# Optimization experiments

Hardware: AMD Instinct MI355X
Metric: run time of the kernel (lower is better)

## Reference

```python
import jax, jax.numpy as jnp
import numpy as np

# Qwen3.5 GatedDeltaNet dims
B, T, HID = 2, 2048, 2048
HK, HV, DK, DV, KW = 16, 32, 128, 128, 4   # k-heads, v-heads, head dims, conv kernel
R = HV // HK                                # GQA repeat factor = 2
KEY_DIM = HK * DK                           # 2048
VAL_DIM = HV * DV                           # 4096
CONV_DIM = 2 * KEY_DIM + VAL_DIM            # 8192
EPS = 1e-6


def setup_inputs() -> dict:
    key = jax.random.key(0)
    ks = jax.random.split(key, 10)
    w = lambda k, shape, s=0.02: (jax.random.normal(k, shape) * s).astype(jnp.float32)
    A = jax.random.uniform(ks[8], (HV,), minval=1e-3, maxval=16.0)
    return {
        "hidden_states": jax.random.normal(ks[0], (B, T, HID), jnp.float32),
        "W_qkv": w(ks[1], (HID, CONV_DIM)),
        "W_z": w(ks[2], (HID, VAL_DIM)),
        "W_b": w(ks[3], (HID, HV)),
        "W_a": w(ks[4], (HID, HV)),
        "conv_w": w(ks[5], (CONV_DIM, KW), 0.5),   # depthwise causal conv taps
        "dt_bias": jnp.ones((HV,), jnp.float32),
        "A_log": jnp.log(A).astype(jnp.float32),
        "norm_weight": jnp.ones((DV,), jnp.float32),
        "W_out": w(ks[9], (VAL_DIM, HID)),
    }


def _forward(hidden_states, W_qkv, W_z, W_b, W_a, conv_w, dt_bias, A_log, norm_weight, W_out):
    x = hidden_states
    # --- projections ---
    qkv = x @ W_qkv                                    # [B,T,CONV_DIM]
    z = x @ W_z                                        # [B,T,VAL_DIM]
    beta = jax.nn.sigmoid(x @ W_b)                     # [B,T,HV]
    alpha = x @ W_a                                    # [B,T,HV]
    g = -jnp.exp(A_log) * jax.nn.softplus(alpha + dt_bias)  # [B,T,HV] (log-decay <= 0)

    # --- fix_query_key_value_ordering: per-k-head interleaved layout ---
    qkv = qkv.reshape(B, T, HK, 2 * DK + R * DV)
    q, k, v = jnp.split(qkv, [DK, 2 * DK], axis=3)
    mixed = jnp.concatenate([q.reshape(B, T, -1), k.reshape(B, T, -1), v.reshape(B, T, -1)], axis=-1)

    # --- causal depthwise short conv (kernel 4) + SiLU ---
    xp = jnp.pad(mixed, ((0, 0), (KW - 1, 0), (0, 0)))
    conv = sum(conv_w[:, i] * xp[:, i:i + T, :] for i in range(KW))
    conv = jax.nn.silu(conv)

    q, k, v = jnp.split(conv, [KEY_DIM, 2 * KEY_DIM], axis=-1)
    q = q.reshape(B, T, HK, DK)
    k = k.reshape(B, T, HK, DK)
    v = v.reshape(B, T, HV, DV)
    gate = z.reshape(B, T, HV, DV)

    # GQA: repeat q,k heads to match v heads
    q = jnp.repeat(q, R, axis=2)                       # [B,T,HV,DK]
    k = jnp.repeat(k, R, axis=2)

    # l2-norm q,k (use_qk_l2norm_in_kernel=True) and default scale 1/sqrt(DK)
    q = q / jnp.sqrt(jnp.sum(q * q, axis=-1, keepdims=True) + 1e-6)
    k = k / jnp.sqrt(jnp.sum(k * k, axis=-1, keepdims=True) + 1e-6)
    q = q * (DK ** -0.5)

    # --- gated delta rule recurrence (scan over time) ---
    # state S: [B,HV,DK,DV];  S_t = a_t*S_{t-1} + k_t (beta_t*(v_t - (a_t*S_{t-1})^T k_t))^T
    def step(S, inp):
        qt, kt, vt, gt, bt = inp                       # [B,HV,DK],[B,HV,DK],[B,HV,DV],[B,HV],[B,HV]
        S = S * jnp.exp(gt)[:, :, None, None]
        kv = jnp.einsum('bhk,bhkv->bhv', kt, S)
        delta = bt[..., None] * (vt - kv)              # [B,HV,DV]
        S = S + kt[..., None] * delta[:, :, None, :]
        o = jnp.einsum('bhk,bhkv->bhv', qt, S)
        return S, o

    tfirst = lambda a: jnp.moveaxis(a, 1, 0)           # [T,B,...]
    S0 = jnp.zeros((B, HV, DK, DV), q.dtype)
    _, o = jax.lax.scan(step, S0, (tfirst(q), tfirst(k), tfirst(v), tfirst(g), tfirst(beta)))
    o = jnp.moveaxis(o, 0, 1)                          # [B,T,HV,DV]

    # --- gated RMSNorm: rmsnorm(o) * silu(gate) * weight ---
    var = jnp.mean(o * o, axis=-1, keepdims=True)
    o = o * jax.lax.rsqrt(var + EPS)
    o = o * jax.nn.silu(gate)
    o = o * norm_weight

    return o.reshape(B, T, VAL_DIM) @ W_out            # [B,T,HID]


def reference(hidden_states, W_qkv, W_z, W_b, W_a, conv_w, dt_bias, A_log, norm_weight, W_out):
    return _forward(hidden_states, W_qkv, W_z, W_b, W_a, conv_w, dt_bias, A_log, norm_weight, W_out)
```

## Files before the change

kernel.cpp:

```cpp
#include <hip/hip_runtime.h>


#define T_LEN 2048
#define MROWS 4096

typedef __bf16 bf16x8 __attribute__((ext_vector_type(8)));
typedef float f32x4 __attribute__((ext_vector_type(4)));

#define MFMA(a, b, c) __builtin_amdgcn_mfma_f32_16x16x32_bf16((a), (b), (c), 0, 0, 0)

__device__ __forceinline__ unsigned short f2bf(float f) {
  unsigned int u = __float_as_uint(f);
  unsigned int r = (u + 0x7fffu + ((u >> 16) & 1u)) >> 16;
  return (unsigned short)r;
}
__device__ __forceinline__ float bf2f(unsigned short u) {
  return __uint_as_float(((unsigned int)u) << 16);
}
__device__ __forceinline__ void gload_lds16(const void* g, void* l) {
  __builtin_amdgcn_global_load_lds(
      (const __attribute__((address_space(1))) unsigned int*)g,
      (__attribute__((address_space(3))) unsigned int*)l, 16, 0, 0);
}

__global__ __launch_bounds__(256) void transpose_f2b(const float* __restrict__ src,
                                                     unsigned short* __restrict__ dst,
                                                     int R, int C) {
  __shared__ float tile[32][33];
  int tx = threadIdx.x & 31, ty = threadIdx.x >> 5;
  int c0 = blockIdx.x * 32, r0 = blockIdx.y * 32;
  #pragma unroll
  for (int i = ty; i < 32; i += 8)
    tile[i][tx] = src[(size_t)(r0 + i) * C + c0 + tx];
  __syncthreads();
  #pragma unroll
  for (int i = ty; i < 32; i += 8)
    dst[(size_t)(c0 + i) * R + r0 + tx] = f2bf(tile[tx][i]);
}

__global__ __launch_bounds__(256) void transpose_multi(const float* __restrict__ Wqkv,
                                                       const float* __restrict__ Wz,
                                                       const float* __restrict__ Wb,
                                                       const float* __restrict__ Wa,
                                                       const float* __restrict__ x,
                                                       unsigned short* __restrict__ WallT,
                                                       unsigned short* __restrict__ WbaT,
                                                       unsigned short* __restrict__ x_bf) {
  int bid = blockIdx.x;
  if (bid >= 24704) {
    int i = (bid - 24704) * 256 + threadIdx.x;
    float4 v = ((const float4*)x)[i];
    ushort4 o;
    o.x = f2bf(v.x); o.y = f2bf(v.y); o.z = f2bf(v.z); o.w = f2bf(v.w);
    ((ushort4*)x_bf)[i] = o;
    return;
  }
  const float* src; unsigned short* dst; int C, cx, ry;
  if (bid < 16384)                 { src = Wqkv; dst = WallT; C = 8192; cx = bid & 255; ry = bid >> 8; }
  else if ((bid -= 16384) < 8192)  { src = Wz; dst = WallT + (size_t)8192 * 2048; C = 4096; cx = bid & 127; ry = bid >> 7; }
  else if ((bid -= 8192) < 64)     { src = Wb; dst = WbaT; C = 32; cx = 0; ry = bid; }
  else { bid -= 64;                  src = Wa; dst = WbaT + (size_t)32 * 2048; C = 32; cx = 0; ry = bid; }
  const int R = 2048;
  __shared__ float tile[32][33];
  int tx = threadIdx.x & 31, ty = threadIdx.x >> 5;
  int c0 = cx * 32, r0 = ry * 32;
  #pragma unroll
  for (int i = ty; i < 32; i += 8)
    if (c0 + tx < C) tile[i][tx] = src[(size_t)(r0 + i) * C + c0 + tx];
  __syncthreads();
  #pragma unroll
  for (int i = ty; i < 32; i += 8)
    if (c0 + i < C) dst[(size_t)(c0 + i) * R + r0 + tx] = f2bf(tile[tx][i]);
}

template <int OUTBF>
__global__ __launch_bounds__(512, 2) void gemm8p(const unsigned short* __restrict__ A, int lda,
                                                 const unsigned short* __restrict__ Bt, int ldb,
                                                 void* __restrict__ Cv, int ldc,
                                                 int Nsplit, void* __restrict__ Cv2, int ldc2,
                                                 int M, int N, int K) {
  __shared__ unsigned short lds[65536];

  const int mtiles = M >> 8;
  const int nwg = gridDim.x, orig = blockIdx.x;
  const int q = nwg >> 3, r = nwg & 7;
  const int xcd = orig & 7, idx = orig >> 3;
  const int swz = (xcd < r ? xcd * (q + 1) : r * (q + 1) + (xcd - r) * q) + idx;
  const int m0 = (swz % mtiles) * 256;
  const int n0 = (swz / mtiles) * 256;

  const int tid = threadIdx.x, lane = tid & 63, wv = tid >> 6;
  const int wm = wv >> 2, wn = wv & 3;
  const int l15 = lane & 15, l4 = lane >> 4;

  f32x4 acc[8][4];
  #pragma unroll
  for (int i = 0; i < 8; i++)
    #pragma unroll
    for (int j = 0; j < 4; j++) acc[i][j] = f32x4{0.f, 0.f, 0.f, 0.f};

  const int NT = K >> 6;

  auto SHALF = [&](int t, int op, int h) {
    unsigned short* base = lds + (t & 1) * 32768 + op * 16384 + h * 8192;
    const unsigned short* G = op ? Bt : A;
    const int ld = op ? ldb : lda;
    const int r0g = (op ? n0 : m0) + h * 128;
    const int k0 = t << 6;
    #pragma unroll
    for (int is = 0; is < 2; is++) {
      int ow = is * 8192 + wv * 1024;
      int o = ow + lane * 16;
      int row = o >> 7, colB = o & 127;
      int scol = colB ^ ((row & 7) << 4);
      gload_lds16(G + (size_t)(r0g + row) * ld + k0 + (scol >> 1), base + (ow >> 1));
    }
  };

  bf16x8 aF[4][2], bF[2][2];
  auto RD_A = [&](int t, int qm) {
    const unsigned short* base = lds + (t & 1) * 32768 + qm * 8192;
    #pragma unroll
    for (int mi = 0; mi < 4; mi++) {
      int ra = wm * 64 + mi * 16 + l15;
      int sw = (ra & 7) << 4;
      #pragma unroll
      for (int kh = 0; kh < 2; kh++) {
        int colB = kh * 64 + l4 * 16;
        aF[mi][kh] = *(const bf16x8*)(base + ra * 64 + ((colB ^ sw) >> 1));
      }
    }
  };
  auto RD_B = [&](int t, int qn) {
    const unsigned short* base = lds + (t & 1) * 32768 + 16384 + qn * 8192;
    #pragma unroll
    for (int ni = 0; ni < 2; ni++) {
      int rb = wn * 32 + ni * 16 + l15;
      int sw = (rb & 7) << 4;
      #pragma unroll
      for (int kh = 0; kh < 2; kh++) {
        int colB = kh * 64 + l4 * 16;
        bF[ni][kh] = *(const bf16x8*)(base + rb * 64 + ((colB ^ sw) >> 1));
      }
    }
  };
  auto COMPUTE = [&](int qm, int qn) {
    __builtin_amdgcn_s_setprio(1);
    #pragma unroll
    for (int mi = 0; mi < 4; mi++)
      #pragma unroll
      for (int ni = 0; ni < 2; ni++)
        #pragma unroll
        for (int kh = 0; kh < 2; kh++)
          acc[qm * 4 + mi][qn * 2 + ni] =
              MFMA(aF[mi][kh], bF[ni][kh], acc[qm * 4 + mi][qn * 2 + ni]);
    __builtin_amdgcn_s_setprio(0);
  };
  auto SBAR = [&]() {
    __builtin_amdgcn_sched_barrier(0);
    __builtin_amdgcn_s_barrier();
    __builtin_amdgcn_sched_barrier(0);
  };

  SHALF(0, 0, 0); SHALF(0, 1, 0); SHALF(0, 1, 1); SHALF(0, 0, 1);
  asm volatile("s_waitcnt vmcnt(4)" ::: "memory");
  SBAR();

  for (int t = 0; t < NT; t++) {
    const bool lastT = (t + 1 >= NT);
    RD_A(t, 0); RD_B(t, 0);
    if (!lastT) SHALF(t + 1, 0, 0);
    COMPUTE(0, 0);
    if (!lastT) asm volatile("s_waitcnt vmcnt(4)" ::: "memory");
    else        asm volatile("s_waitcnt vmcnt(2)" ::: "memory");
    SBAR();
    RD_B(t, 1);
    if (!lastT) SHALF(t + 1, 1, 0);
    COMPUTE(0, 1);
    if (!lastT) asm volatile("s_waitcnt vmcnt(4)" ::: "memory");
    else        asm volatile("s_waitcnt vmcnt(0)" ::: "memory");
    SBAR();
    RD_A(t, 1);
    if (!lastT) SHALF(t + 1, 1, 1);
    COMPUTE(1, 1);
    RD_B(t, 0);
    if (!lastT) SHALF(t + 1, 0, 1);
    COMPUTE(1, 0);
    if (!lastT) {
      asm volatile("s_waitcnt vmcnt(4)" ::: "memory");
      SBAR();
    }
  }

  #pragma unroll
  for (int i = 0; i < 8; i++) {
    int grow = m0 + (i >> 2) * 128 + wm * 64 + (i & 3) * 16 + l4 * 4;
    #pragma unroll
    for (int j = 0; j < 4; j++) {
      int gcol = n0 + (j >> 1) * 128 + wn * 32 + (j & 1) * 16 + l15;
      if (OUTBF) {
        if (gcol < Nsplit) {
          unsigned short* cp = (unsigned short*)Cv + (size_t)grow * ldc + gcol;
          #pragma unroll
          for (int rr = 0; rr < 4; rr++) cp[(size_t)rr * ldc] = f2bf(acc[i][j][rr]);
        } else {
          unsigned short* cp = (unsigned short*)Cv2 + (size_t)grow * ldc2 + (gcol - Nsplit);
          #pragma unroll
          for (int rr = 0; rr < 4; rr++) cp[(size_t)rr * ldc2] = f2bf(acc[i][j][rr]);
        }
      } else {
        float* cp = (float*)Cv + (size_t)grow * ldc + gcol;
        #pragma unroll
        for (int rr = 0; rr < 4; rr++) cp[(size_t)rr * ldc] = acc[i][j][rr];
      }
    }
  }
}

template <int OUTBF, int BN>
__global__ __launch_bounds__(512, 2) void gemm256(const unsigned short* __restrict__ A, int lda,
                                                  const unsigned short* __restrict__ Bt, int ldb,
                                                  void* __restrict__ Cv, int ldc,
                                                  int M, int N, int K) {
  constexpr int BUFSZ = 16384 + BN * 64;
  constexpr int BISS = BN / 64;
  constexpr int IS = 4 + BISS;
  constexpr int WMv = (BN == 256) ? 2 : 4;
  constexpr int MSUB = 256 / (WMv * 16);
  constexpr int MSPAN = 256 / WMv;

  __shared__ unsigned short lds[2 * BUFSZ];

  const int mtiles = M >> 8;
  const int nwg = gridDim.x;
  const int orig = blockIdx.x;
  const int q = nwg >> 3, r = nwg & 7;
  const int xcd = orig & 7, idx = orig >> 3;
  const int swz = (xcd < r ? xcd * (q + 1) : r * (q + 1) + (xcd - r) * q) + idx;
  const int m0 = (swz % mtiles) * 256;
  const int n0 = (swz / mtiles) * BN;

  const int tid = threadIdx.x, lane = tid & 63, wv = tid >> 6;
  const int wm = (BN == 256) ? (wv >> 2) : (wv >> 1);
  const int wn = (BN == 256) ? (wv & 3) : (wv & 1);
  const int l15 = lane & 15, l4 = lane >> 4;

  f32x4 acc[MSUB][4];
  #pragma unroll
  for (int i = 0; i < MSUB; i++)
    #pragma unroll
    for (int j = 0; j < 4; j++) acc[i][j] = f32x4{0.f, 0.f, 0.f, 0.f};

  const int NT = K >> 6;

  auto STAGE = [&](int kt) {
    unsigned short* base = lds + (kt & 1) * BUFSZ;
    const int k0 = kt << 6;
    #pragma unroll
    for (int is = 0; is < 4; is++) {
      int ow = is * 8192 + wv * 1024;
      int o = ow + lane * 16;
      int row = o >> 7, colB = o & 127;
      int scol = colB ^ ((row & 7) << 4);
      gload_lds16(A + (size_t)(m0 + row) * lda + k0 + (scol >> 1), base + (ow >> 1));
    }
    #pragma unroll
    for (int is = 0; is < BISS; is++) {
      int ow = is * 8192 + wv * 1024;
      int o = ow + lane * 16;
      int row = o >> 7, colB = o & 127;
      int scol = colB ^ ((row & 7) << 4);
      gload_lds16(Bt + (size_t)(n0 + row) * ldb + k0 + (scol >> 1), base + 16384 + (ow >> 1));
    }
  };

  STAGE(0);
  if (NT > 1) STAGE(1);
  if constexpr (IS == 8) asm volatile("s_waitcnt vmcnt(8)" ::: "memory");
  else                   asm volatile("s_waitcnt vmcnt(6)" ::: "memory");
  __builtin_amdgcn_sched_barrier(0);
  __builtin_amdgcn_s_barrier();
  __builtin_amdgcn_sched_barrier(0);

  for (int t = 0; t < NT; t++) {
    const unsigned short* Abuf = lds + (t & 1) * BUFSZ;
    const unsigned short* Bbuf = Abuf + 16384;
    bf16x8 bF[4][2];
    #pragma unroll
    for (int n = 0; n < 4; n++) {
      int rb = wn * 64 + n * 16 + l15;
      int sw = (rb & 7) << 4;
      #pragma unroll
      for (int ks = 0; ks < 2; ks++) {
        int colB = (ks * 32 + l4 * 8) * 2;
        bF[n][ks] = *(const bf16x8*)(Bbuf + rb * 64 + ((colB ^ sw) >> 1));
      }
    }
    __builtin_amdgcn_s_setprio(1);
    #pragma unroll
    for (int m = 0; m < MSUB; m++) {
      int ra = wm * MSPAN + m * 16 + l15;
      int sw = (ra & 7) << 4;
      int c0b = l4 * 16;
      bf16x8 a0 = *(const bf16x8*)(Abuf + ra * 64 + ((c0b ^ sw) >> 1));
      bf16x8 a1 = *(const bf16x8*)(Abuf + ra * 64 + (((64 + c0b) ^ sw) >> 1));
      #pragma unroll
      for (int n = 0; n < 4; n++) {
        acc[m][n] = MFMA(a0, bF[n][0], acc[m][n]);
        acc[m][n] = MFMA(a1, bF[n][1], acc[m][n]);
      }
    }
    __builtin_amdgcn_s_setprio(0);
    __builtin_amdgcn_sched_barrier(0);
    __builtin_amdgcn_s_barrier();
    __builtin_amdgcn_sched_barrier(0);
    if (t + 2 < NT) STAGE(t + 2);
    if (t + 1 < NT) {
      if (t + 2 < NT) {
        if constexpr (IS == 8) asm volatile("s_waitcnt vmcnt(8)" ::: "memory");
        else                   asm volatile("s_waitcnt vmcnt(6)" ::: "memory");
      } else {
        asm volatile("s_waitcnt vmcnt(0)" ::: "memory");
      }
      __builtin_amdgcn_sched_barrier(0);
      __builtin_amdgcn_s_barrier();
      __builtin_amdgcn_sched_barrier(0);
    }
  }

  #pragma unroll
  for (int m = 0; m < MSUB; m++) {
    int grow = m0 + wm * MSPAN + m * 16 + l4 * 4;
    #pragma unroll
    for (int n = 0; n < 4; n++) {
      int gcol = n0 + wn * 64 + n * 16 + l15;
      if (OUTBF) {
        unsigned short* cp = (unsigned short*)Cv + (size_t)grow * ldc + gcol;
        #pragma unroll
        for (int rr = 0; rr < 4; rr++) cp[(size_t)rr * ldc] = f2bf(acc[m][n][rr]);
      } else {
        float* cp = (float*)Cv + (size_t)grow * ldc + gcol;
        #pragma unroll
        for (int rr = 0; rr < 4; rr++) cp[(size_t)rr * ldc] = acc[m][n][rr];
      }
    }
  }
}

__global__ __launch_bounds__(256) void gemm_ba(const unsigned short* __restrict__ A, int lda,
                                               const unsigned short* __restrict__ Bt, int ldb,
                                               const float* __restrict__ A_log,
                                               const float* __restrict__ dt_bias,
                                               unsigned short* __restrict__ betab,
                                               float* __restrict__ g,
                                               int M, int K) {
  __shared__ unsigned short As[128 * 64];
  __shared__ unsigned short Bs[128 * 64];
  const int tid = threadIdx.x, lane = tid & 63, wv = tid >> 6;
  const int wr = wv >> 1, wc = wv & 1;
  const int m0 = blockIdx.y * 128, n0 = 0;
  const int lrow8 = lane >> 3;
  const int lk8 = (lane & 7) * 8;

  f32x4 acc[4][4];
  #pragma unroll
  for (int i = 0; i < 4; i++)
    #pragma unroll
    for (int j = 0; j < 4; j++) acc[i][j] = f32x4{0.f, 0.f, 0.f, 0.f};

  for (int k0 = 0; k0 < K; k0 += 64) {
    #pragma unroll
    for (int j = 0; j < 4; ++j) {
      int chunk = j * 4 + wv;
      int r = chunk * 8 + lrow8;
      gload_lds16(A + (size_t)(m0 + r) * lda + k0 + lk8, (void*)(As + chunk * 512));
      gload_lds16(Bt + (size_t)(n0 + r) * ldb + k0 + lk8, (void*)(Bs + chunk * 512));
    }
    __syncthreads();
    #pragma unroll
    for (int half = 0; half < 2; ++half) {
      int ko = half * 32 + (lane >> 4) * 8;
      bf16x8 af[4], bfr[4];
      #pragma unroll
      for (int i = 0; i < 4; i++) {
        int ra = wr * 64 + i * 16 + (lane & 15);
        af[i] = *(const bf16x8*)(As + ra * 64 + ko);
        int rb = wc * 64 + i * 16 + (lane & 15);
        bfr[i] = *(const bf16x8*)(Bs + rb * 64 + ko);
      }
      #pragma unroll
      for (int i = 0; i < 4; i++)
        #pragma unroll
        for (int j = 0; j < 4; j++)
          acc[i][j] = MFMA(af[i], bfr[j], acc[i][j]);
    }
    __syncthreads();
  }
  int cr4 = (lane >> 4) * 4;
  int cc = lane & 15;
  #pragma unroll
  for (int i = 0; i < 4; i++) {
    int row = m0 + wr * 64 + i * 16 + cr4;
    #pragma unroll
    for (int j = 0; j < 4; j++) {
      int col = wc * 64 + j * 16 + cc;
      if (col < 64) {
        #pragma unroll
        for (int r = 0; r < 4; r++) {
          int erow = row + r;
          float a = acc[i][j][r];
          if (col < 32) {
            betab[(size_t)erow * 32 + col] = f2bf(1.f / (1.f + expf(-a)));
          } else {
            int hvv = col - 32;
            float xg = a + dt_bias[hvv];
            float sp = (xg > 20.f) ? xg : log1pf(expf(xg));
            g[(size_t)erow * 32 + hvv] = -expf(A_log[hvv]) * sp;
          }
        }
      }
    }
  }
}

__global__ __launch_bounds__(256) void conv_kernel(const unsigned short* __restrict__ qkv,
                                                   const float* __restrict__ conv_w,
                                                   unsigned short* __restrict__ out) {
  const int seg = blockIdx.x, tt = blockIdx.y, b = blockIdx.z;
  const int tid = threadIdx.x;
  const int c0 = seg * 128;
  const bool isq = seg < 16;
  int scb;
  if (isq) scb = seg * 512;
  else if (seg < 32) scb = (seg - 16) * 512 + 128;
  else scb = ((seg - 32) >> 1) * 512 + 256 + ((seg - 32) & 1) * 128;

  __shared__ unsigned short raw[35][136];
  __shared__ float cw[4][132];

  for (int i = tid; i < 512; i += 256) {
    int cl = i >> 2, tap = i & 3;
    cw[tap][cl] = conv_w[(size_t)(c0 + cl) * 4 + tap];
  }
  const int t0 = tt * 32;
  for (int i = tid; i < 560; i += 256) {
    int row = i >> 4, col = (i & 15) * 8;
    int gt = t0 - 3 + row;
    uint4 v = make_uint4(0u, 0u, 0u, 0u);
    if (gt >= 0) v = *(const uint4*)(qkv + (size_t)(b * T_LEN + gt) * 8192 + scb + col);
    *(uint4*)(&raw[row][col]) = v;
  }
  __syncthreads();
  const int s = tid >> 3, dg = tid & 7;
  union RawU { uint4 v[2]; unsigned short h[16]; };
  RawU u[4];
  #pragma unroll
  for (int i = 0; i < 4; i++) {
    const uint4* p = (const uint4*)&raw[s + i][dg * 16];
    u[i].v[0] = p[0]; u[i].v[1] = p[1];
  }
  float vals[16]; float ss = 0.f;
  #pragma unroll
  for (int j = 0; j < 16; j++) {
    float a = 0.f;
    #pragma unroll
    for (int i = 0; i < 4; i++) a = fmaf(cw[i][dg * 16 + j], bf2f(u[i].h[j]), a);
    a = a / (1.f + expf(-a));
    vals[j] = a; ss += a * a;
  }
  if (seg < 32) {
    ss += __shfl_xor(ss, 1); ss += __shfl_xor(ss, 2); ss += __shfl_xor(ss, 4);
    float sc = rsqrtf(ss + 1e-6f);
    if (isq) sc *= 0.08838834764831845f;
    #pragma unroll
    for (int j = 0; j < 16; j++) vals[j] *= sc;
  }
  union { uint4 v[2]; unsigned short h[16]; } ov;
  #pragma unroll
  for (int j = 0; j < 16; j++) ov.h[j] = f2bf(vals[j]);
  unsigned short* op = out + (size_t)(b * T_LEN + t0 + s) * 8192 + c0 + dg * 16;
  *(uint4*)(op) = ov.v[0];
  *(uint4*)(op + 8) = ov.v[1];
}

__global__ __launch_bounds__(256) void prep_kernel(const unsigned short* __restrict__ conv,
                                                   const float* __restrict__ g,
                                                   const unsigned short* __restrict__ betab,
                                                   unsigned short* __restrict__ M1g,
                                                   unsigned short* __restrict__ M2g,
                                                   unsigned char* __restrict__ vecs) {
  const int c = blockIdx.x, bh = blockIdx.y;
  const int b = bh >> 5, hv = bh & 31, hk = hv >> 1;
  const int bhc = bh * 32 + c;
  const int tid = threadIdx.x, lane = tid & 63, wv = tid >> 6;
  const int r0 = b * T_LEN + c * 64;
  const int l15 = lane & 15, l4 = lane >> 4;

  __shared__ unsigned short Kb[128 * 72];
  __shared__ unsigned short QbX[64 * 136];
  __shared__ unsigned short Lbf[64 * 72];
  __shared__ unsigned short Pb[64 * 72];
  __shared__ unsigned short WT[3 * 16 * 40];
  __shared__ float Gs[64], SCs[64], BLs[64];

  unsigned short* Qb = QbX;
  unsigned short* XTb = QbX;
  unsigned short* Xdrow = QbX + 4608;

  if (wv == 0) {
    float gt = g[(size_t)(r0 + lane) * 32 + hv];
    #pragma unroll
    for (int d = 1; d < 64; d <<= 1) {
      float o = __shfl_up(gt, (unsigned)d, 64);
      if (lane >= d) gt += o;
    }
    float GC = __shfl(gt, 63, 64);
    float lam = expf(gt);
    float beta = bf2f(betab[(size_t)(r0 + lane) * 32 + hv]);
    Gs[lane] = gt;
    SCs[lane] = expf(GC - gt);
    BLs[lane] = beta;
    unsigned short* vb16 = (unsigned short*)(vecs + (size_t)bhc * 272);
    vb16[lane] = f2bf(beta * lam);
    vb16[64 + lane] = f2bf(lam);
    if (lane == 0) *(float*)(vecs + (size_t)bhc * 272 + 256) = expf(GC);
  }
  const unsigned short* Kg = conv + (size_t)r0 * 8192 + 2048 + hk * 128;
  const unsigned short* Qg = conv + (size_t)r0 * 8192 + hk * 128;
  for (int u = tid; u < 1024; u += 256) {
    int row = u >> 4, col = (u & 15) * 8;
    *(uint4*)(&Kb[row * 136 + col]) = *(const uint4*)(Kg + (size_t)row * 8192 + col);
    *(uint4*)(&Qb[row * 136 + col]) = *(const uint4*)(Qg + (size_t)row * 8192 + col);
  }
  __syncthreads();

  {
    f32x4 akk[4], aqk[4];
    #pragma unroll
    for (int st = 0; st < 4; st++) { akk[st] = f32x4{0,0,0,0}; aqk[st] = f32x4{0,0,0,0}; }
    int trow = wv * 16 + l15;
    int klo = l4 * 8;
    #pragma unroll
    for (int ks = 0; ks < 4; ks++) {
      int ko = ks * 32 + klo;
      bf16x8 ak = *(const bf16x8*)(&Kb[trow * 136 + ko]);
      bf16x8 aq = *(const bf16x8*)(&Qb[trow * 136 + ko]);
      #pragma unroll
      for (int st = 0; st < 4; st++) {
        bf16x8 bk = *(const bf16x8*)(&Kb[(st * 16 + l15) * 136 + ko]);
        akk[st] = MFMA(ak, bk, akk[st]);
        aqk[st] = MFMA(aq, bk, aqk[st]);
      }
    }
    int orow = wv * 16 + l4 * 4;
    int oc = l15;
    #pragma unroll
    for (int st = 0; st < 4; st++)
      #pragma unroll
      for (int r = 0; r < 4; r++) {
        int t = orow + r, ssv = st * 16 + oc;
        float e = expf(fminf(Gs[t] - Gs[ssv], 0.f));
        Lbf[t * 72 + ssv] = f2bf((ssv < t) ? BLs[t] * e * akk[st][r] : 0.f);
        Pb[t * 72 + ssv] = f2bf((ssv <= t) ? e * aqk[st][r] : 0.f);
      }
  }
  __syncthreads();

  unsigned short ktv[32];
  {
    int dk = tid >> 1, tb = (tid & 1) * 32;
    #pragma unroll
    for (int i = 0; i < 32; i++)
      ktv[i] = f2bf(bf2f(Kb[(tb + i) * 136 + dk]) * SCs[tb + i]);
    for (int u = tid; u < 896; u += 256) {
      *(uint4*)(&QbX[u * 8]) = make_uint4(0u, 0u, 0u, 0u);
    }
    for (int u = tid; u < 240; u += 256) {
      *(uint4*)(&WT[u * 8]) = make_uint4(0u, 0u, 0u, 0u);
    }
  }
  __syncthreads();

  {
    int dk = tid >> 1, tb = (tid & 1) * 32;
    #pragma unroll
    for (int i = 0; i < 32; i++) Kb[dk * 72 + tb + i] = ktv[i];
  }
  {
    const int w16 = wv * 16;
    const int cc = l15;
    float xr[16];
    #pragma unroll
    for (int t = 0; t < 16; t++) {
      float acc = (cc == t) ? 1.f : 0.f;
      union { uint4 v[2]; unsigned short h[16]; } rw;
      const uint4* p = (const uint4*)(&Lbf[(w16 + t) * 72 + w16]);
      rw.v[0] = p[0]; rw.v[1] = p[1];
      #pragma unroll
      for (int s = 0; s < 16; s++) {
        if (s < t) acc = fmaf(-bf2f(rw.h[s]), xr[s], acc);
      }
      xr[t] = acc;
    }
    if (lane < 16) {
      #pragma unroll
      for (int t = 0; t < 16; t++) {
        unsigned short v = f2bf(xr[t]);
        XTb[(w16 + cc) * 72 + w16 + t] = v;
        Xdrow[wv * 640 + t * 40 + cc] = v;
      }
    }
  }
  __syncthreads();

  if (wv < 3) {
    const int j = wv;
    for (int i = j + 1; i < 4; i++) {
      f32x4 w_ = f32x4{0.f, 0.f, 0.f, 0.f};
      #pragma unroll
      for (int ks = 0; ks < 2; ks++) {
        int so = ks * 32 + l4 * 8;
        bf16x8 af = *(const bf16x8*)(&Lbf[(i * 16 + l15) * 72 + so]);
        bf16x8 bfv = *(const bf16x8*)(&XTb[(j * 16 + l15) * 72 + so]);
        w_ = MFMA(af, bfv, w_);
      }
      #pragma unroll
      for (int r = 0; r < 4; r++)
        WT[j * 640 + l15 * 40 + l4 * 4 + r] = f2bf(-w_[r]);
      f32x4 xij = f32x4{0.f, 0.f, 0.f, 0.f};
      {
        bf16x8 af = *(const bf16x8*)(&Xdrow[i * 640 + l15 * 40 + l4 * 8]);
        bf16x8 bfv = *(const bf16x8*)(&WT[j * 640 + l15 * 40 + l4 * 8]);
        xij = MFMA(af, bfv, xij);
      }
      #pragma unroll
      for (int r = 0; r < 4; r++)
        XTb[(j * 16 + l15) * 72 + i * 16 + l4 * 4 + r] = f2bf(xij[r]);
    }
  }
  __syncthreads();

  for (int tt = wv * 12; tt < wv * 12 + 12; tt++) {
    f32x4 acc = f32x4{0, 0, 0, 0};
    const unsigned short* Abase;
    int mrow, jc;
    if (tt < 16) { mrow = (tt >> 2) * 16; jc = (tt & 3) * 16; Abase = Pb + mrow * 72; }
    else { int i2 = tt - 16; mrow = (i2 >> 2) * 16; jc = (i2 & 3) * 16; Abase = Kb + mrow * 72; }
    #pragma unroll
    for (int ks = 0; ks < 2; ks++) {
      int so = ks * 32 + l4 * 8;
      bf16x8 af = *(const bf16x8*)(Abase + l15 * 72 + so);
      bf16x8 bfv = *(const bf16x8*)(&XTb[(jc + l15) * 72 + so]);
      acc = MFMA(af, bfv, acc);
    }
    int ro = mrow + l4 * 4, co = jc + l15;
    if (tt < 16) {
      #pragma unroll
      for (int r = 0; r < 4; r++)
        M1g[(size_t)bhc * 4096 + (ro + r) * 64 + co] = f2bf(acc[r]);
    } else {
      #pragma unroll
      for (int r = 0; r < 4; r++)
        M2g[(size_t)bhc * 8192 + (ro + r) * 64 + co] = f2bf(acc[r]);
    }
  }
}

__global__ __launch_bounds__(512) void seq_kernel(unsigned short* __restrict__ conv,
                                                  const unsigned short* __restrict__ M1g,
                                                  const unsigned short* __restrict__ M2g,
                                                  const unsigned char* __restrict__ vecs,
                                                  const unsigned short* __restrict__ betab) {
  const int dvh = blockIdx.x * 64;
  const int bh = blockIdx.y;
  const int b = bh >> 5, hv = bh & 31, hk = hv >> 1;
  const int tid = threadIdx.x, lane = tid & 63, wv = tid >> 6;
  const int l15 = lane & 15, l4 = lane >> 4;

  __shared__ unsigned short Kb[64 * 136], Qb[64 * 136];
  __shared__ unsigned short Vb[64 * 72];
  __shared__ unsigned short S0T[64 * 136];
  __shared__ unsigned short rhsT[64 * 72];
  __shared__ unsigned short bts[64];

  f32x4 S[4];
  #pragma unroll
  for (int i = 0; i < 4; i++) S[i] = f32x4{0.f, 0.f, 0.f, 0.f};

  for (int i = tid; i < 1088; i += 512) *(uint4*)(&S0T[i * 8]) = make_uint4(0u, 0u, 0u, 0u);
  __syncthreads();

  const int trt = (wv >> 1) * 16;
  const int dsb = (wv & 1) * 32;
  const int dkb = wv * 16;

  for (int c = 0; c < 32; c++) {
    const int r0 = b * T_LEN + c * 64;
    const int bhc = bh * 32 + c;
    const unsigned char* vb = vecs + (size_t)bhc * 272;
    const unsigned short* vb16 = (const unsigned short*)vb;
    #pragma unroll
    for (int j = 0; j < 2; j++) {
      int u = j * 512 + tid;
      int row = u >> 4, col = (u & 15) * 8;
      uint4 kv = *(const uint4*)(conv + (size_t)(r0 + row) * 8192 + 2048 + hk * 128 + col);
      uint4 qv = *(const uint4*)(conv + (size_t)(r0 + row) * 8192 + hk * 128 + col);
      *(uint4*)(&Kb[row * 136 + col]) = kv;
      float lam = bf2f(vb16[64 + row]);
      union { uint4 u4; unsigned short h[8]; } qq; qq.u4 = qv;
      #pragma unroll
      for (int e = 0; e < 8; e++) qq.h[e] = f2bf(bf2f(qq.h[e]) * lam);
      *(uint4*)(&Qb[row * 136 + col]) = qq.u4;
    }
    {
      int row = tid >> 3, col = (tid & 7) * 8;
      *(uint4*)(&Vb[row * 72 + col]) =
          *(const uint4*)(conv + (size_t)(r0 + row) * 8192 + 4096 + hv * 128 + dvh + col);
      if (tid < 64) bts[tid] = betab[(size_t)(r0 + tid) * 32 + hv];
    }
    __syncthreads();
    #pragma unroll
    for (int dt = 0; dt < 2; dt++) {
      int dv0 = dsb + dt * 16;
      f32x4 acc = f32x4{0, 0, 0, 0};
      #pragma unroll
      for (int ks = 0; ks < 4; ks++) {
        int ko = ks * 32 + l4 * 8;
        bf16x8 af = *(const bf16x8*)(&Kb[(trt + l15) * 136 + ko]);
        bf16x8 bfv = *(const bf16x8*)(&S0T[(dv0 + l15) * 136 + ko]);
        acc = MFMA(af, bfv, acc);
      }
      #pragma unroll
      for (int r = 0; r < 4; r++) {
        int tl = trt + l4 * 4 + r;
        float beta = bf2f(bts[tl]);
        float bl = bf2f(vb16[tl]);
        float vv = bf2f(Vb[tl * 72 + dv0 + l15]);
        rhsT[(dv0 + l15) * 72 + tl] = f2bf(beta * vv - bl * acc[r]);
      }
    }
    __syncthreads();
    {
      const unsigned short* m1b = M1g + (size_t)bhc * 4096;
      #pragma unroll
      for (int dt = 0; dt < 2; dt++) {
        int dv0 = dsb + dt * 16;
        f32x4 acc = f32x4{0, 0, 0, 0};
        #pragma unroll
        for (int ks = 0; ks < 2; ks++) {
          int so = ks * 32 + l4 * 8;
          union { uint4 u4; bf16x8 h; } af;
          af.u4 = *(const uint4*)(m1b + (trt + l15) * 64 + so);
          bf16x8 bfv = *(const bf16x8*)(&rhsT[(dv0 + l15) * 72 + so]);
          acc = MFMA(af.h, bfv, acc);
        }
        #pragma unroll
        for (int ks = 0; ks < 4; ks++) {
          int ko = ks * 32 + l4 * 8;
          bf16x8 af = *(const bf16x8*)(&Qb[(trt + l15) * 136 + ko]);
          bf16x8 bfv = *(const bf16x8*)(&S0T[(dv0 + l15) * 136 + ko]);
          acc = MFMA(af, bfv, acc);
        }
        #pragma unroll
        for (int r = 0; r < 4; r++) {
          int t = r0 + trt + l4 * 4 + r;
          conv[(size_t)t * 8192 + 4096 + hv * 128 + dvh + dv0 + l15] = f2bf(acc[r]);
        }
      }
      float lamC = *(const float*)(vb + 256);
      const unsigned short* m2b = M2g + (size_t)bhc * 8192;
      #pragma unroll
      for (int dvt = 0; dvt < 4; dvt++) {
        f32x4 a = S[dvt];
        a[0] *= lamC; a[1] *= lamC; a[2] *= lamC; a[3] *= lamC;
        #pragma unroll
        for (int ks = 0; ks < 2; ks++) {
          int so = ks * 32 + l4 * 8;
          union { uint4 u4; bf16x8 h; } af;
          af.u4 = *(const uint4*)(m2b + (dkb + l15) * 64 + so);
          bf16x8 bfv = *(const bf16x8*)(&rhsT[(dvt * 16 + l15) * 72 + so]);
          a = MFMA(af.h, bfv, a);
        }
        S[dvt] = a;
      }
    }
    __syncthreads();
    #pragma unroll
    for (int dvt = 0; dvt < 4; dvt++)
      #pragma unroll
      for (int r = 0; r < 4; r++)
        S0T[(dvt * 16 + l15) * 136 + dkb + l4 * 4 + r] = f2bf(S[dvt][r]);
  }
}

__global__ __launch_bounds__(256) void rmsgate_kernel(unsigned short* __restrict__ conv,
                                                      const unsigned short* __restrict__ zg,
                                                      const float* __restrict__ nw) {
  int wid = blockIdx.x * 4 + (threadIdx.x >> 6);
  int lane = threadIdx.x & 63;
  int row = wid >> 5, hv = wid & 31;
  unsigned short* op = conv + (size_t)row * 8192 + 4096 + hv * 128;
  float o0 = bf2f(op[lane]), o1 = bf2f(op[64 + lane]);
  float ss = o0 * o0 + o1 * o1;
  #pragma unroll
  for (int m = 1; m < 64; m <<= 1) ss += __shfl_xor(ss, m);
  float r = rsqrtf(ss * (1.f / 128.f) + 1e-6f);
  const unsigned short* zp = zg + (size_t)row * 4096 + hv * 128;
  float g0 = bf2f(zp[lane]), g1 = bf2f(zp[64 + lane]);
  g0 = g0 / (1.f + expf(-g0));
  g1 = g1 / (1.f + expf(-g1));
  op[lane] = f2bf(o0 * r * g0 * nw[lane]);
  op[64 + lane] = f2bf(o1 * r * g1 * nw[64 + lane]);
}

extern "C" void kernel_launch(void* const* d_in, const int* in_sizes, int n_in,
                              void* d_out, int out_size, void* d_ws, size_t ws_size,
                              hipStream_t stream) {
  (void)in_sizes; (void)n_in; (void)out_size;
  const float* x       = (const float*)d_in[0];
  const float* W_qkv   = (const float*)d_in[1];
  const float* W_z     = (const float*)d_in[2];
  const float* W_b     = (const float*)d_in[3];
  const float* W_a     = (const float*)d_in[4];
  const float* conv_w  = (const float*)d_in[5];
  const float* dt_bias = (const float*)d_in[6];
  const float* A_log   = (const float*)d_in[7];
  const float* nw      = (const float*)d_in[8];
  const float* W_out   = (const float*)d_in[9];
  float* out = (float*)d_out;

  const size_t NEED = 169115648ULL;
  if (ws_size < NEED) return;

  char* ws = (char*)d_ws;
  unsigned short* WbaT   = (unsigned short*)(ws + 0);
  unsigned short* qkv_bf = (unsigned short*)(ws + 0);
  unsigned short* M1g    = (unsigned short*)(ws + 0);
  unsigned short* M2g    = (unsigned short*)(ws + 16777216);
  unsigned short* WoutT  = (unsigned short*)(ws + 0);
  unsigned short* zg     = (unsigned short*)(ws + 67108864);
  unsigned short* WallT  = (unsigned short*)(ws + 100663296);
  unsigned short* x_bf   = (unsigned short*)(ws + 100663296 + 50331648);
  unsigned short* convb  = (unsigned short*)(ws + 100663296);
  unsigned short* betab  = (unsigned short*)(ws + 167772160);
  float* gbuf            = (float*)(ws + 168034304);
  unsigned char* vecs    = (unsigned char*)(ws + 168558592);

  const int M = MROWS;

  transpose_multi<<<32896, 256, 0, stream>>>(W_qkv, W_z, W_b, W_a, x, WallT, WbaT, x_bf);

  gemm_ba<<<dim3(1, M / 128), 256, 0, stream>>>(x_bf, 2048, WbaT, 2048,
                                                A_log, dt_bias, betab, gbuf, M, 2048);

  gemm8p<1><<<768, 512, 0, stream>>>(x_bf, 2048, WallT, 2048,
                                     qkv_bf, 8192, 8192, zg, 4096, M, 12288, 2048);

  conv_kernel<<<dim3(64, 64, 2), 256, 0, stream>>>(qkv_bf, conv_w, convb);

  prep_kernel<<<dim3(32, 64), 256, 0, stream>>>(convb, gbuf, betab, M1g, M2g, vecs);

  seq_kernel<<<dim3(2, 64), 512, 0, stream>>>(convb, M1g, M2g, vecs, betab);

  rmsgate_kernel<<<32768, 256, 0, stream>>>(convb, zg, nw);

  transpose_f2b<<<dim3(2048 / 32, 4096 / 32), 256, 0, stream>>>(W_out, WoutT, 4096, 2048);
  gemm256<0, 128><<<256, 512, 0, stream>>>(convb + 4096, 8192, WoutT, 4096, out, 2048, M, 2048, 4096);
}
```

Before: 597.5 us.

## Double-buffer and register-prefetch next chunk's Q/K/V in sequential scan kernel

The sequential chunk-recurrence kernel now issues the global loads for the next chunk's K, Q, V and beta into registers at the start of each iteration. It writes them into a second LDS buffer after the state update, so load latency overlaps with the MFMA work of the current chunk. The per-chunk sync moves to the end of the loop, and the first chunk is loaded in a prologue. This costs extra LDS (doubled K/Q/V buffers) and more registers, which could lower occupancy. It also tidies an unused n0 offset in gemm_ba.

Measured after the change: 602.7 us. About the same (+0.9%).

```diff
diff --git a/kernel.cpp b/kernel.cpp
--- a/kernel.cpp
+++ b/kernel.cpp
@@ -358,7 +358,7 @@
   __shared__ unsigned short Bs[128 * 64];
   const int tid = threadIdx.x, lane = tid & 63, wv = tid >> 6;
   const int wr = wv >> 1, wc = wv & 1;
-  const int m0 = blockIdx.y * 128, n0 = 0;
+  const int m0 = blockIdx.y * 128;
   const int lrow8 = lane >> 3;
   const int lk8 = (lane & 7) * 8;
 
@@ -374,7 +374,7 @@
       int chunk = j * 4 + wv;
       int r = chunk * 8 + lrow8;
       gload_lds16(A + (size_t)(m0 + r) * lda + k0 + lk8, (void*)(As + chunk * 512));
-      gload_lds16(Bt + (size_t)(n0 + r) * ldb + k0 + lk8, (void*)(Bs + chunk * 512));
+      gload_lds16(Bt + (size_t)r * ldb + k0 + lk8, (void*)(Bs + chunk * 512));
     }
     __syncthreads();
     #pragma unroll
@@ -677,17 +677,40 @@
   const int tid = threadIdx.x, lane = tid & 63, wv = tid >> 6;
   const int l15 = lane & 15, l4 = lane >> 4;
 
-  __shared__ unsigned short Kb[64 * 136], Qb[64 * 136];
-  __shared__ unsigned short Vb[64 * 72];
+  __shared__ unsigned short Kb[2][64 * 136], Qb[2][64 * 136];
+  __shared__ unsigned short Vb[2][64 * 72];
   __shared__ unsigned short S0T[64 * 136];
   __shared__ unsigned short rhsT[64 * 72];
-  __shared__ unsigned short bts[64];
+  __shared__ unsigned short bts[2][64];
 
   f32x4 S[4];
   #pragma unroll
   for (int i = 0; i < 4; i++) S[i] = f32x4{0.f, 0.f, 0.f, 0.f};
 
   for (int i = tid; i < 1088; i += 512) *(uint4*)(&S0T[i * 8]) = make_uint4(0u, 0u, 0u, 0u);
+
+  const int srow = tid >> 4, scol = (tid & 15) * 8;
+  const int vrow = tid >> 3, vcol = (tid & 7) * 8;
+
+  {
+    const int r0 = b * T_LEN;
+    const unsigned short* vb16n = (const unsigned short*)(vecs + (size_t)(bh * 32) * 272);
+    #pragma unroll
+    for (int j = 0; j < 2; j++) {
+      int row = srow + j * 32;
+      uint4 kv = *(const uint4*)(conv + (size_t)(r0 + row) * 8192 + 2048 + hk * 128 + scol);
+      uint4 qv = *(const uint4*)(conv + (size_t)(r0 + row) * 8192 + hk * 128 + scol);
+      *(uint4*)(&Kb[0][row * 136 + scol]) = kv;
+      float lam = bf2f(vb16n[64 + row]);
+      union { uint4 u4; unsigned short h[8]; } qq; qq.u4 = qv;
+      #pragma unroll
+      for (int e = 0; e < 8; e++) qq.h[e] = f2bf(bf2f(qq.h[e]) * lam);
+      *(uint4*)(&Qb[0][row * 136 + scol]) = qq.u4;
+    }
+    *(uint4*)(&Vb[0][vrow * 72 + vcol]) =
+        *(const uint4*)(conv + (size_t)(r0 + vrow) * 8192 + 4096 + hv * 128 + dvh + vcol);
+    if (tid < 64) bts[0][tid] = betab[(size_t)(r0 + tid) * 32 + hv];
+  }
   __syncthreads();
 
   const int trt = (wv >> 1) * 16;
@@ -695,30 +718,29 @@
   const int dkb = wv * 16;
 
   for (int c = 0; c < 32; c++) {
+    const int cur = c & 1;
     const int r0 = b * T_LEN + c * 64;
     const int bhc = bh * 32 + c;
     const unsigned char* vb = vecs + (size_t)bhc * 272;
     const unsigned short* vb16 = (const unsigned short*)vb;
-    #pragma unroll
-    for (int j = 0; j < 2; j++) {
-      int u = j * 512 + tid;
-      int row = u >> 4, col = (u & 15) * 8;
-      uint4 kv = *(const uint4*)(conv + (size_t)(r0 + row) * 8192 + 2048 + hk * 128 + col);
-      uint4 qv = *(const uint4*)(conv + (size_t)(r0 + row) * 8192 + hk * 128 + col);
-      *(uint4*)(&Kb[row * 136 + col]) = kv;
-      float lam = bf2f(vb16[64 + row]);
-      union { uint4 u4; unsigned short h[8]; } qq; qq.u4 = qv;
-      #pragma unroll
-      for (int e = 0; e < 8; e++) qq.h[e] = f2bf(bf2f(qq.h[e]) * lam);
-      *(uint4*)(&Qb[row * 136 + col]) = qq.u4;
-    }
-    {
-      int row = tid >> 3, col = (tid & 7) * 8;
-      *(uint4*)(&Vb[row * 72 + col]) =
-          *(const uint4*)(conv + (size_t)(r0 + row) * 8192 + 4096 + hv * 128 + dvh + col);
-      if (tid < 64) bts[tid] = betab[(size_t)(r0 + tid) * 32 + hv];
-    }
-    __syncthreads();
+
+    uint4 kpre0 = make_uint4(0u, 0u, 0u, 0u), kpre1 = kpre0;
+    uint4 qpre0 = kpre0, qpre1 = kpre0, vpre = kpre0;
+    float lam0 = 0.f, lam1 = 0.f;
+    unsigned short btpre = 0;
+    if (c + 1 < 32) {
+      const int r1 = r0 + 64;
+      const unsigned short* vb16n = (const unsigned short*)(vecs + (size_t)(bhc + 1) * 272);
+      kpre0 = *(const uint4*)(conv + (size_t)(r1 + srow) * 8192 + 2048 + hk * 128 + scol);
+      qpre0 = *(const uint4*)(conv + (size_t)(r1 + srow) * 8192 + hk * 128 + scol);
+      kpre1 = *(const uint4*)(conv + (size_t)(r1 + srow + 32) * 8192 + 2048 + hk * 128 + scol);
+      qpre1 = *(const uint4*)(conv + (size_t)(r1 + srow + 32) * 8192 + hk * 128 + scol);
+      vpre  = *(const uint4*)(conv + (size_t)(r1 + vrow) * 8192 + 4096 + hv * 128 + dvh + vcol);
+      lam0 = bf2f(vb16n[64 + srow]);
+      lam1 = bf2f(vb16n[64 + srow + 32]);
+      if (tid < 64) btpre = betab[(size_t)(r1 + tid) * 32 + hv];
+    }
+
     #pragma unroll
     for (int dt = 0; dt < 2; dt++) {
       int dv0 = dsb + dt * 16;
@@ -726,16 +748,16 @@
       #pragma unroll
       for (int ks = 0; ks < 4; ks++) {
         int ko = ks * 32 + l4 * 8;
-        bf16x8 af = *(const bf16x8*)(&Kb[(trt + l15) * 136 + ko]);
+        bf16x8 af = *(const bf16x8*)(&Kb[cur][(trt + l15) * 136 + ko]);
         bf16x8 bfv = *(const bf16x8*)(&S0T[(dv0 + l15) * 136 + ko]);
         acc = MFMA(af, bfv, acc);
       }
       #pragma unroll
       for (int r = 0; r < 4; r++) {
         int tl = trt + l4 * 4 + r;
-        float beta = bf2f(bts[tl]);
+        float beta = bf2f(bts[cur][tl]);
         float bl = bf2f(vb16[tl]);
-        float vv = bf2f(Vb[tl * 72 + dv0 + l15]);
+        float vv = bf2f(Vb[cur][tl * 72 + dv0 + l15]);
         rhsT[(dv0 + l15) * 72 + tl] = f2bf(beta * vv - bl * acc[r]);
       }
     }
@@ -757,7 +779,7 @@
         #pragma unroll
         for (int ks = 0; ks < 4; ks++) {
           int ko = ks * 32 + l4 * 8;
-          bf16x8 af = *(const bf16x8*)(&Qb[(trt + l15) * 136 + ko]);
+          bf16x8 af = *(const bf16x8*)(&Qb[cur][(trt + l15) * 136 + ko]);
           bf16x8 bfv = *(const bf16x8*)(&S0T[(dv0 + l15) * 136 + ko]);
           acc = MFMA(af, bfv, acc);
         }
@@ -790,6 +812,23 @@
       #pragma unroll
       for (int r = 0; r < 4; r++)
         S0T[(dvt * 16 + l15) * 136 + dkb + l4 * 4 + r] = f2bf(S[dvt][r]);
+    if (c + 1 < 32) {
+      int nxt = cur ^ 1;
+      union { uint4 u4; unsigned short h[8]; } qq;
+      *(uint4*)(&Kb[nxt][srow * 136 + scol]) = kpre0;
+      qq.u4 = qpre0;
+      #pragma unroll
+      for (int e = 0; e < 8; e++) qq.h[e] = f2bf(bf2f(qq.h[e]) * lam0);
+      *(uint4*)(&Qb[nxt][srow * 136 + scol]) = qq.u4;
+      *(uint4*)(&Kb[nxt][(srow + 32) * 136 + scol]) = kpre1;
+      qq.u4 = qpre1;
+      #pragma unroll
+      for (int e = 0; e < 8; e++) qq.h[e] = f2bf(bf2f(qq.h[e]) * lam1);
+      *(uint4*)(&Qb[nxt][(srow + 32) * 136 + scol]) = qq.u4;
+      *(uint4*)(&Vb[nxt][vrow * 72 + vcol]) = vpre;
+      if (tid < 64) bts[nxt][tid] = btpre;
+    }
+    __syncthreads();
   }
 }
 
```
